# Kernel optimization log

Measured on AMD Instinct MI355X. Metric: run time of the kernel, lower is better.

## Reference

```python
import jax, jax.numpy as jnp
import numpy as np

NH = 8       # num_heads
EDIM = 256   # embedding_dim (also per-head dim in this module)
BS, SQL = 4, 1024


def setup_inputs() -> dict:
    key = jax.random.key(0)
    ks = jax.random.split(key, 5)
    scale_in = 1.0 / np.sqrt(EDIM)
    scale_out = 1.0 / np.sqrt(NH * EDIM)
    return {
        "x": jax.random.normal(ks[0], (BS, SQL, EDIM), dtype=jnp.float32),
        "w_attn": jax.random.normal(ks[1], (NH * 3 * EDIM, EDIM), dtype=jnp.float32) * scale_in,
        "b_attn": jax.random.normal(ks[2], (NH * 3 * EDIM,), dtype=jnp.float32) * scale_in,
        "w_out": jax.random.normal(ks[3], (EDIM, NH * EDIM), dtype=jnp.float32) * scale_out,
        "b_out": jax.random.normal(ks[4], (EDIM,), dtype=jnp.float32) * scale_out,
    }


def reference(x, w_attn, b_attn, w_out, b_out):
    bs, sql, edim = x.shape
    nh = NH
    # projections: (bs, sql, nh*3*edim); split into Q, K, V chunks of nh*edim
    proj = x @ w_attn.T + b_attn
    q, k, v = jnp.split(proj, 3, axis=-1)
    # Faithful to torch: raw view (bs, sql, nh*edim) -> (bs, nh, sql, edim),
    # a reinterpretation of memory, NOT a transpose.
    q = q.reshape(bs, nh, sql, edim)
    k = k.reshape(bs, nh, sql, edim)
    v = v.reshape(bs, nh, sql, edim)
    # scaled dot-product scores: (bs, nh, sql, sql)
    scores = jnp.einsum("bhqd,bhkd->bhqk", q, k) / jnp.sqrt(jnp.float32(edim))
    # causal mask: -inf strictly above the diagonal (equivalent to adding triu(-inf, 1))
    causal = jnp.tril(jnp.ones((sql, sql), dtype=bool))
    scores = jnp.where(causal, scores, -jnp.inf)
    attn = jax.nn.softmax(scores, axis=-1)
    out = jnp.einsum("bhqk,bhkd->bhqd", attn, v)
    # Faithful raw view back: (bs, nh, sql, edim) -> (bs, sql, nh*edim)
    out = out.reshape(bs, sql, nh * edim)
    return out @ w_out.T + b_out
```

## Files before the change

### kernel.cpp

```cpp
#include <hip/hip_runtime.h>

#define SQL  1024
#define EDIM 256
#define NHD  8
#define NKV  (NHD * 3 * EDIM)
#define MROWS (4 * SQL)

typedef short bf16x8 __attribute__((ext_vector_type(8)));
typedef float f32x4 __attribute__((ext_vector_type(4)));

__device__ __forceinline__ unsigned short f2bf(float f) {
  unsigned u = __float_as_uint(f);
  u += 0x7fff + ((u >> 16) & 1);
  return (unsigned short)(u >> 16);
}

__device__ __forceinline__ void g2lds16(const void* g, void* l) {
  __builtin_amdgcn_global_load_lds(
      (const __attribute__((address_space(1))) unsigned int*)g,
      (__attribute__((address_space(3))) unsigned int*)l, 16, 0, 0);
}

__device__ __forceinline__ void storev(float* p, float v) { *p = v; }
__device__ __forceinline__ void storev(unsigned short* p, float v) { *p = f2bf(v); }

__global__ __launch_bounds__(256) void cast_bf16(
    const float* __restrict__ in, unsigned short* __restrict__ out, int n8) {
  int i = blockIdx.x * 256 + threadIdx.x;
  if (i >= n8) return;
  float4 a = ((const float4*)in)[2 * i];
  float4 b = ((const float4*)in)[2 * i + 1];
  union { unsigned short s[8]; ulonglong2 v; } u;
  u.s[0] = f2bf(a.x); u.s[1] = f2bf(a.y); u.s[2] = f2bf(a.z); u.s[3] = f2bf(a.w);
  u.s[4] = f2bf(b.x); u.s[5] = f2bf(b.y); u.s[6] = f2bf(b.z); u.s[7] = f2bf(b.w);
  ((ulonglong2*)out)[i] = u.v;
}

template <int BM, int BN, typename OutT>
__global__ __launch_bounds__(256) void gemm_mfma(
    const unsigned short* __restrict__ A, const unsigned short* __restrict__ B,
    const float* __restrict__ bias, OutT* __restrict__ C,
    int M, int N, int K) {
  constexpr int TM = BM / 32, TN = BN / 32;
  __shared__ __align__(16) unsigned short As[2][BM * 32];
  __shared__ __align__(16) unsigned short Bs[2][BN * 32];
  const int tid = threadIdx.x;
  const int wave = tid >> 6, lane = tid & 63;
  const int quad = lane >> 4, l16 = lane & 15;
  const int wm = (wave >> 1) * (BM / 2), wn = (wave & 1) * (BN / 2);
  const int m0 = blockIdx.x * BM, n0 = blockIdx.y * BN;
  const int sw = (l16 >> 1) & 3;

  f32x4 acc[TM][TN];
  #pragma unroll
  for (int i = 0; i < TM; i++)
    #pragma unroll
    for (int j = 0; j < TN; j++) acc[i][j] = {0.f, 0.f, 0.f, 0.f};

  auto stage = [&](int k0, int bb) {
    #pragma unroll
    for (int it = 0; it < BM / 64; it++) {
      int flat = it * 256 + tid;
      int row = flat >> 2;
      int cg = (flat & 3) ^ ((row >> 1) & 3);
      g2lds16(A + (size_t)(m0 + row) * K + k0 + cg * 8, &As[bb][flat * 8]);
    }
    #pragma unroll
    for (int it = 0; it < BN / 64; it++) {
      int flat = it * 256 + tid;
      int row = flat >> 2;
      int cg = (flat & 3) ^ ((row >> 1) & 3);
      g2lds16(B + (size_t)(n0 + row) * K + k0 + cg * 8, &Bs[bb][flat * 8]);
    }
  };

  stage(0, 0);
  __syncthreads();
  for (int k0 = 0; k0 < K; k0 += 32) {
    const int bb = (k0 >> 5) & 1;
    if (k0 + 32 < K) stage(k0 + 32, bb ^ 1);
    bf16x8 af[TM], bf[TN];
    #pragma unroll
    for (int i = 0; i < TM; i++)
      af[i] = *(const bf16x8*)&As[bb][(wm + i * 16 + l16) * 32 + (quad ^ sw) * 8];
    #pragma unroll
    for (int j = 0; j < TN; j++)
      bf[j] = *(const bf16x8*)&Bs[bb][(wn + j * 16 + l16) * 32 + (quad ^ sw) * 8];
    #pragma unroll
    for (int i = 0; i < TM; i++)
      #pragma unroll
      for (int j = 0; j < TN; j++)
        acc[i][j] = __builtin_amdgcn_mfma_f32_16x16x32_bf16(af[i], bf[j], acc[i][j], 0, 0, 0);
    __syncthreads();
  }

  #pragma unroll
  for (int i = 0; i < TM; i++) {
    #pragma unroll
    for (int r = 0; r < 4; r++) {
      int m = m0 + wm + i * 16 + quad * 4 + r;
      #pragma unroll
      for (int j = 0; j < TN; j++) {
        int n = n0 + wn + j * 16 + l16;
        storev(&C[(size_t)m * N + n], acc[i][j][r] + bias[n]);
      }
    }
  }
}

__global__ __launch_bounds__(256) void transpose_v(
    const unsigned short* __restrict__ proj, unsigned short* __restrict__ vt) {
  __shared__ unsigned short T[64][66];
  const int tid = threadIdx.x;
  const int s0 = blockIdx.x * 64, d0 = blockIdx.y * 64, bh = blockIdx.z;
  const int b = bh >> 3, h = bh & 7;
  #pragma unroll
  for (int it = 0; it < 2; it++) {
    int c = it * 256 + tid;
    int sr = c >> 3, k8 = (c & 7) * 8;
    int s = s0 + sr;
    const unsigned short* src = proj + (size_t)(b * SQL + h * 128 + (s >> 3)) * NKV
                                + 2 * 2048 + (s & 7) * 256 + d0 + k8;
    *(ulonglong2*)&T[sr][k8] = *(const ulonglong2*)src;
  }
  __syncthreads();
  #pragma unroll
  for (int it = 0; it < 2; it++) {
    int c = it * 256 + tid;
    int dr = c >> 3, s8 = (c & 7) * 8;
    unsigned short tmp[8];
    #pragma unroll
    for (int j = 0; j < 8; j++) tmp[j] = T[s8 + j][dr];
    unsigned short* dst = vt + ((size_t)bh * EDIM + d0 + dr) * SQL + s0 + s8;
    *(ulonglong2*)dst = *(ulonglong2*)tmp;
  }
}

__global__ __launch_bounds__(256) void attn_mfma(
    const unsigned short* __restrict__ proj,
    const unsigned short* __restrict__ vt,
    unsigned short* __restrict__ oflat) {
  __shared__ __align__(16) unsigned short lds[35328];
  unsigned short* Ps = lds + 32768;

  const int tid = threadIdx.x;
  const int wave = tid >> 6, lane = tid & 63;
  const int quad = lane >> 4, l16 = lane & 15;
  const int slot = blockIdx.x & 255, round = blockIdx.x >> 8;
  const int bh = slot & 31;
  const int j = slot >> 5;
  const int qt = round ? j : 15 - j;
  const int b = bh >> 3, h = bh & 7;
  const int q0 = qt * 64;

  #pragma unroll
  for (int it = 0; it < 8; it++) {
    int c = it * 256 + tid;
    int r = c >> 5, ch = (c & 31) ^ (r & 7);
    int s = q0 + r;
    g2lds16(proj + (size_t)(b * SQL + h * 128 + (s >> 3)) * NKV + (s & 7) * 256 + ch * 8,
            lds + c * 8);
  }
  __syncthreads();
  bf16x8 aq[8];
  const int qrow = wave * 16 + l16;
  #pragma unroll
  for (int kk = 0; kk < 8; kk++)
    aq[kk] = *(const bf16x8*)&lds[qrow * 256 + ((kk * 4 + quad) ^ (qrow & 7)) * 8];
  __syncthreads();

  f32x4 o[16];
  #pragma unroll
  for (int t = 0; t < 16; t++) o[t] = {0.f, 0.f, 0.f, 0.f};
  float l_r[4] = {0.f, 0.f, 0.f, 0.f};

  auto stage = [&](int kt, int bb) {
    unsigned short* KsB = lds + bb * 16384;
    unsigned short* VtB = KsB + 8192;
    #pragma unroll
    for (int it = 0; it < 4; it++) {
      int c = it * 256 + tid;
      int r = c >> 5, ch = (c & 31) ^ (r & 7);
      int s = kt * 32 + r;
      g2lds16(proj + (size_t)(b * SQL + h * 128 + (s >> 3)) * NKV + 2048 + (s & 7) * 256 + ch * 8,
              KsB + c * 8);
    }
    #pragma unroll
    for (int it = 0; it < 4; it++) {
      int c = it * 256 + tid;
      int d = c >> 2, ch = (c & 3) ^ (d & 3);
      g2lds16(vt + ((size_t)bh * EDIM + d) * SQL + kt * 32 + ch * 8, VtB + c * 8);
    }
  };

  const int nkt = 2 * qt + 2;
  stage(0, 0);
  __syncthreads();

  for (int kt = 0; kt < nkt; kt++) {
    const int bb = kt & 1;
    if (kt + 1 < nkt) stage(kt + 1, bb ^ 1);
    const unsigned short* KsB = lds + bb * 16384;
    const unsigned short* VtB = KsB + 8192;

    f32x4 s0 = {0.f, 0.f, 0.f, 0.f}, s1 = {0.f, 0.f, 0.f, 0.f};
    #pragma unroll
    for (int kk = 0; kk < 8; kk++) {
      int ch = (kk * 4 + quad) ^ (l16 & 7);
      bf16x8 b0 = *(const bf16x8*)&KsB[l16 * 256 + ch * 8];
      bf16x8 b1 = *(const bf16x8*)&KsB[(16 + l16) * 256 + ch * 8];
      s0 = __builtin_amdgcn_mfma_f32_16x16x32_bf16(aq[kk], b0, s0, 0, 0, 0);
      s1 = __builtin_amdgcn_mfma_f32_16x16x32_bf16(aq[kk], b1, s1, 0, 0, 0);
    }

    const int kg0 = kt * 32 + l16, kg1 = kg0 + 16;
    #pragma unroll
    for (int r = 0; r < 4; r++) {
      int qg = q0 + wave * 16 + quad * 4 + r;
      float p0 = (kg0 <= qg) ? __expf(s0[r] * 0.0625f) : 0.f;
      float p1 = (kg1 <= qg) ? __expf(s1[r] * 0.0625f) : 0.f;
      l_r[r] += p0 + p1;
      Ps[(wave * 16 + quad * 4 + r) * 40 + l16]      = f2bf(p0);
      Ps[(wave * 16 + quad * 4 + r) * 40 + 16 + l16] = f2bf(p1);
    }

    bf16x8 ap = *(const bf16x8*)&Ps[(wave * 16 + l16) * 40 + quad * 8];
    #pragma unroll
    for (int t = 0; t < 16; t++) {
      bf16x8 bv = *(const bf16x8*)&VtB[(t * 16 + l16) * 32 + (quad ^ (l16 & 3)) * 8];
      o[t] = __builtin_amdgcn_mfma_f32_16x16x32_bf16(ap, bv, o[t], 0, 0, 0);
    }
    __syncthreads();
  }

  #pragma unroll
  for (int r = 0; r < 4; r++) {
    float l = l_r[r];
    #pragma unroll
    for (int off = 1; off < 16; off <<= 1) l += __shfl_xor(l, off);
    float inv = 1.0f / l;
    int s = q0 + wave * 16 + quad * 4 + r;
    unsigned short* dst = oflat + (size_t)(b * SQL + h * 128 + (s >> 3)) * 2048 + (s & 7) * 256;
    #pragma unroll
    for (int t = 0; t < 16; t++)
      dst[t * 16 + l16] = f2bf(o[t][r] * inv);
  }
}

extern "C" void kernel_launch(void* const* d_in, const int* in_sizes, int n_in,
                              void* d_out, int out_size, void* d_ws, size_t ws_size,
                              hipStream_t stream) {
  const float* x      = (const float*)d_in[0];
  const float* w_attn = (const float*)d_in[1];
  const float* b_attn = (const float*)d_in[2];
  const float* w_out  = (const float*)d_in[3];
  const float* b_out  = (const float*)d_in[4];
  float* out = (float*)d_out;

  char* p = (char*)d_ws;
  unsigned short* proj = (unsigned short*)p;  p += (size_t)MROWS * NKV * 2;
  unsigned short* obf  = (unsigned short*)p;  p += (size_t)MROWS * 2048 * 2;
  unsigned short* vtb  = (unsigned short*)p;  p += (size_t)32 * EDIM * SQL * 2;
  unsigned short* xb   = (unsigned short*)p;  p += (size_t)MROWS * EDIM * 2;
  unsigned short* wb   = (unsigned short*)p;  p += (size_t)NKV * EDIM * 2;
  unsigned short* wob  = (unsigned short*)p;

  cast_bf16<<<(MROWS * EDIM / 8 + 255) / 256, 256, 0, stream>>>(x, xb, MROWS * EDIM / 8);
  cast_bf16<<<(NKV * EDIM / 8 + 255) / 256, 256, 0, stream>>>(w_attn, wb, NKV * EDIM / 8);
  cast_bf16<<<(EDIM * 2048 / 8 + 255) / 256, 256, 0, stream>>>(w_out, wob, EDIM * 2048 / 8);

  gemm_mfma<128, 128, unsigned short><<<dim3(MROWS / 128, NKV / 128), 256, 0, stream>>>(
      xb, wb, b_attn, proj, MROWS, NKV, EDIM);
  transpose_v<<<dim3(SQL / 64, EDIM / 64, 32), 256, 0, stream>>>(proj, vtb);
  attn_mfma<<<512, 256, 0, stream>>>(proj, vtb, obf);
  gemm_mfma<64, 64, float><<<dim3(MROWS / 64, EDIM / 64), 256, 0, stream>>>(
      obf, wob, b_out, out, MROWS, EDIM, NHD * EDIM);
}
```

Measured before the change: 170.9 us.

## Merge cast kernels, vectorize GEMM epilogue, split attention waves over query and dim halves

The three fp32-to-bf16 cast launches become one kernel, which saves launch overhead. The GEMM swaps its MFMA operands so each lane holds 4 consecutive output columns, which allows float4 bias loads and vectorized stores. The attention kernel now assigns each wave a 32-query by 128-dim half of the tile instead of 16 queries by full dim, and it skips fully masked causal key tiles per wave. Row sums are reduced across the wave pairs through LDS. It also uses exp2 with a folded scale, an explicit waitcnt plus barrier, and a launch bound of 2 blocks per SIMD. This adds register pressure and a barrier inside the loop.

```diff
diff --git a/kernel.cpp b/kernel.cpp
--- a/kernel.cpp
+++ b/kernel.cpp
@@ -21,19 +21,28 @@
       (__attribute__((address_space(3))) unsigned int*)l, 16, 0, 0);
 }
 
-__device__ __forceinline__ void storev(float* p, float v) { *p = v; }
-__device__ __forceinline__ void storev(unsigned short* p, float v) { *p = f2bf(v); }
-
-__global__ __launch_bounds__(256) void cast_bf16(
-    const float* __restrict__ in, unsigned short* __restrict__ out, int n8) {
+__device__ __forceinline__ void store4(unsigned short* p, float4 v) {
+  union { unsigned short s[4]; uint2 u; } t;
+  t.s[0] = f2bf(v.x); t.s[1] = f2bf(v.y); t.s[2] = f2bf(v.z); t.s[3] = f2bf(v.w);
+  *(uint2*)p = t.u;
+}
+__device__ __forceinline__ void store4(float* p, float4 v) { *(float4*)p = v; }
+
+__global__ __launch_bounds__(256) void cast3_bf16(
+    const float* __restrict__ s0, unsigned short* __restrict__ d0, int n0,
+    const float* __restrict__ s1, unsigned short* __restrict__ d1, int n1,
+    const float* __restrict__ s2, unsigned short* __restrict__ d2, int n2) {
   int i = blockIdx.x * 256 + threadIdx.x;
-  if (i >= n8) return;
-  float4 a = ((const float4*)in)[2 * i];
-  float4 b = ((const float4*)in)[2 * i + 1];
-  union { unsigned short s[8]; ulonglong2 v; } u;
-  u.s[0] = f2bf(a.x); u.s[1] = f2bf(a.y); u.s[2] = f2bf(a.z); u.s[3] = f2bf(a.w);
-  u.s[4] = f2bf(b.x); u.s[5] = f2bf(b.y); u.s[6] = f2bf(b.z); u.s[7] = f2bf(b.w);
-  ((ulonglong2*)out)[i] = u.v;
+  const float* s; unsigned short* d;
+  if (i < n0) { s = s0; d = d0; }
+  else if (i < n0 + n1) { i -= n0; s = s1; d = d1; }
+  else { i -= n0 + n1; if (i >= n2) return; s = s2; d = d2; }
+  float4 a = ((const float4*)s)[2 * i];
+  float4 b = ((const float4*)s)[2 * i + 1];
+  union { unsigned short u[8]; ulonglong2 v; } t;
+  t.u[0] = f2bf(a.x); t.u[1] = f2bf(a.y); t.u[2] = f2bf(a.z); t.u[3] = f2bf(a.w);
+  t.u[4] = f2bf(b.x); t.u[5] = f2bf(b.y); t.u[6] = f2bf(b.z); t.u[7] = f2bf(b.w);
+  ((ulonglong2*)d)[i] = t.v;
 }
 
 template <int BM, int BN, typename OutT>
@@ -90,20 +99,20 @@
     for (int i = 0; i < TM; i++)
       #pragma unroll
       for (int j = 0; j < TN; j++)
-        acc[i][j] = __builtin_amdgcn_mfma_f32_16x16x32_bf16(af[i], bf[j], acc[i][j], 0, 0, 0);
+        acc[i][j] = __builtin_amdgcn_mfma_f32_16x16x32_bf16(bf[j], af[i], acc[i][j], 0, 0, 0);
     __syncthreads();
   }
 
   #pragma unroll
-  for (int i = 0; i < TM; i++) {
-    #pragma unroll
-    for (int r = 0; r < 4; r++) {
-      int m = m0 + wm + i * 16 + quad * 4 + r;
-      #pragma unroll
-      for (int j = 0; j < TN; j++) {
-        int n = n0 + wn + j * 16 + l16;
-        storev(&C[(size_t)m * N + n], acc[i][j][r] + bias[n]);
-      }
+  for (int j = 0; j < TN; j++) {
+    const int nb = n0 + wn + j * 16 + quad * 4;
+    const float4 bias4 = *(const float4*)&bias[nb];
+    #pragma unroll
+    for (int i = 0; i < TM; i++) {
+      const int m = m0 + wm + i * 16 + l16;
+      float4 v = {acc[i][j][0] + bias4.x, acc[i][j][1] + bias4.y,
+                  acc[i][j][2] + bias4.z, acc[i][j][3] + bias4.w};
+      store4(&C[(size_t)m * N + nb], v);
     }
   }
 }
@@ -136,20 +145,23 @@
   }
 }
 
-__global__ __launch_bounds__(256) void attn_mfma(
+__global__ __launch_bounds__(256, 2) void attn_mfma(
     const unsigned short* __restrict__ proj,
     const unsigned short* __restrict__ vt,
     unsigned short* __restrict__ oflat) {
   __shared__ __align__(16) unsigned short lds[35328];
+  __shared__ float lsum[2][64];
   unsigned short* Ps = lds + 32768;
 
   const int tid = threadIdx.x;
   const int wave = tid >> 6, lane = tid & 63;
   const int quad = lane >> 4, l16 = lane & 15;
+  const int qh = wave >> 1;
+  const int kh = wave & 1;
   const int slot = blockIdx.x & 255, round = blockIdx.x >> 8;
   const int bh = slot & 31;
-  const int j = slot >> 5;
-  const int qt = round ? j : 15 - j;
+  const int jj = slot >> 5;
+  const int qt = round ? jj : 15 - jj;
   const int b = bh >> 3, h = bh & 7;
   const int q0 = qt * 64;
 
@@ -162,17 +174,22 @@
             lds + c * 8);
   }
   __syncthreads();
-  bf16x8 aq[8];
-  const int qrow = wave * 16 + l16;
-  #pragma unroll
-  for (int kk = 0; kk < 8; kk++)
-    aq[kk] = *(const bf16x8*)&lds[qrow * 256 + ((kk * 4 + quad) ^ (qrow & 7)) * 8];
-  __syncthreads();
-
-  f32x4 o[16];
-  #pragma unroll
-  for (int t = 0; t < 16; t++) o[t] = {0.f, 0.f, 0.f, 0.f};
-  float l_r[4] = {0.f, 0.f, 0.f, 0.f};
+  bf16x8 aq[2][8];
+  #pragma unroll
+  for (int qs = 0; qs < 2; qs++) {
+    const int qrow = qh * 32 + qs * 16 + l16;
+    #pragma unroll
+    for (int kk = 0; kk < 8; kk++)
+      aq[qs][kk] = *(const bf16x8*)&lds[qrow * 256 + ((kk * 4 + quad) ^ (qrow & 7)) * 8];
+  }
+  __syncthreads();
+
+  f32x4 o[2][8];
+  #pragma unroll
+  for (int qs = 0; qs < 2; qs++)
+    #pragma unroll
+    for (int tl = 0; tl < 8; tl++) o[qs][tl] = {0.f, 0.f, 0.f, 0.f};
+  float l_r[2][4] = {{0.f, 0.f, 0.f, 0.f}, {0.f, 0.f, 0.f, 0.f}};
 
   auto stage = [&](int kt, int bb) {
     unsigned short* KsB = lds + bb * 16384;
@@ -202,48 +219,67 @@
     if (kt + 1 < nkt) stage(kt + 1, bb ^ 1);
     const unsigned short* KsB = lds + bb * 16384;
     const unsigned short* VtB = KsB + 8192;
-
-    f32x4 s0 = {0.f, 0.f, 0.f, 0.f}, s1 = {0.f, 0.f, 0.f, 0.f};
-    #pragma unroll
-    for (int kk = 0; kk < 8; kk++) {
-      int ch = (kk * 4 + quad) ^ (l16 & 7);
-      bf16x8 b0 = *(const bf16x8*)&KsB[l16 * 256 + ch * 8];
-      bf16x8 b1 = *(const bf16x8*)&KsB[(16 + l16) * 256 + ch * 8];
-      s0 = __builtin_amdgcn_mfma_f32_16x16x32_bf16(aq[kk], b0, s0, 0, 0, 0);
-      s1 = __builtin_amdgcn_mfma_f32_16x16x32_bf16(aq[kk], b1, s1, 0, 0, 0);
-    }
-
-    const int kg0 = kt * 32 + l16, kg1 = kg0 + 16;
+    const bool live = (kt * 32 <= q0 + qh * 32 + 31);
+
+    if (live) {
+      f32x4 s0 = {0.f, 0.f, 0.f, 0.f}, s1 = {0.f, 0.f, 0.f, 0.f};
+      const int krow = kh * 16 + l16;
+      #pragma unroll
+      for (int kk = 0; kk < 8; kk++) {
+        bf16x8 bk = *(const bf16x8*)&KsB[krow * 256 + ((kk * 4 + quad) ^ (krow & 7)) * 8];
+        s0 = __builtin_amdgcn_mfma_f32_16x16x32_bf16(aq[0][kk], bk, s0, 0, 0, 0);
+        s1 = __builtin_amdgcn_mfma_f32_16x16x32_bf16(aq[1][kk], bk, s1, 0, 0, 0);
+      }
+      const int kg = kt * 32 + kh * 16 + l16;
+      #pragma unroll
+      for (int r = 0; r < 4; r++) {
+        const int qg0 = q0 + qh * 32 + quad * 4 + r;
+        float p0 = (kg <= qg0)      ? exp2f(s0[r] * 0.09016844f) : 0.f;
+        float p1 = (kg <= qg0 + 16) ? exp2f(s1[r] * 0.09016844f) : 0.f;
+        l_r[0][r] += p0;
+        l_r[1][r] += p1;
+        Ps[(qh * 32 + quad * 4 + r) * 40 + kh * 16 + l16]        = f2bf(p0);
+        Ps[(qh * 32 + 16 + quad * 4 + r) * 40 + kh * 16 + l16]   = f2bf(p1);
+      }
+    }
+    asm volatile("s_waitcnt lgkmcnt(0)\n\ts_barrier" ::: "memory");
+    if (live) {
+      bf16x8 ap0 = *(const bf16x8*)&Ps[(qh * 32 + l16) * 40 + quad * 8];
+      bf16x8 ap1 = *(const bf16x8*)&Ps[(qh * 32 + 16 + l16) * 40 + quad * 8];
+      #pragma unroll
+      for (int tl = 0; tl < 8; tl++) {
+        const int vrow = kh * 128 + tl * 16 + l16;
+        bf16x8 bv = *(const bf16x8*)&VtB[vrow * 32 + (quad ^ (l16 & 3)) * 8];
+        o[0][tl] = __builtin_amdgcn_mfma_f32_16x16x32_bf16(ap0, bv, o[0][tl], 0, 0, 0);
+        o[1][tl] = __builtin_amdgcn_mfma_f32_16x16x32_bf16(ap1, bv, o[1][tl], 0, 0, 0);
+      }
+    }
+    __syncthreads();
+  }
+
+  #pragma unroll
+  for (int qs = 0; qs < 2; qs++)
     #pragma unroll
     for (int r = 0; r < 4; r++) {
-      int qg = q0 + wave * 16 + quad * 4 + r;
-      float p0 = (kg0 <= qg) ? __expf(s0[r] * 0.0625f) : 0.f;
-      float p1 = (kg1 <= qg) ? __expf(s1[r] * 0.0625f) : 0.f;
-      l_r[r] += p0 + p1;
-      Ps[(wave * 16 + quad * 4 + r) * 40 + l16]      = f2bf(p0);
-      Ps[(wave * 16 + quad * 4 + r) * 40 + 16 + l16] = f2bf(p1);
-    }
-
-    bf16x8 ap = *(const bf16x8*)&Ps[(wave * 16 + l16) * 40 + quad * 8];
-    #pragma unroll
-    for (int t = 0; t < 16; t++) {
-      bf16x8 bv = *(const bf16x8*)&VtB[(t * 16 + l16) * 32 + (quad ^ (l16 & 3)) * 8];
-      o[t] = __builtin_amdgcn_mfma_f32_16x16x32_bf16(ap, bv, o[t], 0, 0, 0);
-    }
-    __syncthreads();
-  }
-
-  #pragma unroll
-  for (int r = 0; r < 4; r++) {
-    float l = l_r[r];
-    #pragma unroll
-    for (int off = 1; off < 16; off <<= 1) l += __shfl_xor(l, off);
-    float inv = 1.0f / l;
-    int s = q0 + wave * 16 + quad * 4 + r;
-    unsigned short* dst = oflat + (size_t)(b * SQL + h * 128 + (s >> 3)) * 2048 + (s & 7) * 256;
-    #pragma unroll
-    for (int t = 0; t < 16; t++)
-      dst[t * 16 + l16] = f2bf(o[t][r] * inv);
+      float l = l_r[qs][r];
+      #pragma unroll
+      for (int off = 1; off < 16; off <<= 1) l += __shfl_xor(l, off);
+      if (l16 == 0) lsum[kh][qh * 32 + qs * 16 + quad * 4 + r] = l;
+    }
+  __syncthreads();
+  #pragma unroll
+  for (int qs = 0; qs < 2; qs++) {
+    #pragma unroll
+    for (int r = 0; r < 4; r++) {
+      const int row = qh * 32 + qs * 16 + quad * 4 + r;
+      const float inv = 1.0f / (lsum[0][row] + lsum[1][row]);
+      const int s = q0 + row;
+      unsigned short* dst = oflat + (size_t)(b * SQL + h * 128 + (s >> 3)) * 2048
+                            + (s & 7) * 256 + kh * 128;
+      #pragma unroll
+      for (int tl = 0; tl < 8; tl++)
+        dst[tl * 16 + l16] = f2bf(o[qs][tl][r] * inv);
+    }
   }
 }
 
@@ -265,9 +301,11 @@
   unsigned short* wb   = (unsigned short*)p;  p += (size_t)NKV * EDIM * 2;
   unsigned short* wob  = (unsigned short*)p;
 
-  cast_bf16<<<(MROWS * EDIM / 8 + 255) / 256, 256, 0, stream>>>(x, xb, MROWS * EDIM / 8);
-  cast_bf16<<<(NKV * EDIM / 8 + 255) / 256, 256, 0, stream>>>(w_attn, wb, NKV * EDIM / 8);
-  cast_bf16<<<(EDIM * 2048 / 8 + 255) / 256, 256, 0, stream>>>(w_out, wob, EDIM * 2048 / 8);
+  const int n0 = MROWS * EDIM / 8;
+  const int n1 = NKV * EDIM / 8;
+  const int n2 = EDIM * 2048 / 8;
+  cast3_bf16<<<(n0 + n1 + n2) / 256, 256, 0, stream>>>(x, xb, n0, w_attn, wb, n1,
+                                                       w_out, wob, n2);
 
   gemm_mfma<128, 128, unsigned short><<<dim3(MROWS / 128, NKV / 128), 256, 0, stream>>>(
       xb, wb, b_attn, proj, MROWS, NKV, EDIM);
```

New measurement: 186.3 us. 1.09x slower.
